# Optimization experiments

Hardware: AMD Instinct MI355X
Metric: run time of the kernel (lower is better)

Reference implementation:

```python
import jax, jax.numpy as jnp
import numpy as np

B, S, H, K = 8, 2048, 768, 128
FILTERS = (1, 3, 5)
C = H // len(FILTERS)  # 256 channels per conv, concat -> H
LN_EPS = 1e-05
COS_EPS = 1e-08


def setup_inputs() -> dict:
    key = jax.random.key(0)
    ks = jax.random.split(key, 16)
    mk = lambda k, shape: jax.random.normal(k, shape, dtype=jnp.float32) * 0.02
    return {
        "representation": jax.random.normal(ks[0], (B, S, H), dtype=jnp.float32),
        "src_mask": jnp.ones((B, S), dtype=jnp.float32),
        # conv weights stored as [k, H_in, C_out] for lax 1D conv (torch Conv2d(1,C,(k,H)))
        "enc_conv_w1": mk(ks[1], (1, H, C)),
        "enc_conv_w3": mk(ks[2], (3, H, C)),
        "enc_conv_w5": mk(ks[3], (5, H, C)),
        "ln_g": jnp.ones((H,), jnp.float32),
        "ln_b": jnp.zeros((H,), jnp.float32),
        "enc_lin_w": mk(ks[4], (H, H)),   # torch Linear weight [out,in]
        "enc_tr_w": mk(ks[5], (K, H)),
        "dec_tr_w": mk(ks[6], (H, K)),
        "dec_conv_w1": mk(ks[7], (1, H, C)),
        "dec_conv_w3": mk(ks[8], (3, H, C)),
        "dec_conv_w5": mk(ks[9], (5, H, C)),
        "dec_lin_w": mk(ks[10], (H, H)),
        "out_lin_w": mk(ks[11], (H, H)),
    }


def _multi_conv(x, ws):
    # x: [B, S, H]; each w: [k, H, C]; torch pads (k//2, 0) -> same-length for odd k
    outs = []
    for w in ws:
        k = w.shape[0]
        outs.append(jax.lax.conv_general_dilated(
            x, w, window_strides=(1,), padding=[(k // 2, k // 2)],
            dimension_numbers=("NWC", "WIO", "NWC")))
    return jnp.concatenate(outs, axis=-1)  # [B, S, H]


def _layernorm(x, g, b):
    mu = jnp.mean(x, axis=-1, keepdims=True)
    var = jnp.mean((x - mu) ** 2, axis=-1, keepdims=True)
    return (x - mu) * jax.lax.rsqrt(var + LN_EPS) * g + b


def reference(representation, src_mask, enc_conv_w1, enc_conv_w3, enc_conv_w5,
              ln_g, ln_b, enc_lin_w, enc_tr_w, dec_tr_w,
              dec_conv_w1, dec_conv_w3, dec_conv_w5, dec_lin_w, out_lin_w):
    # ---- AutoEncoder (dropout layers are identity in eval mode) ----
    h = _multi_conv(representation, (enc_conv_w1, enc_conv_w3, enc_conv_w5))
    h = _layernorm(h + representation, ln_g, ln_b)
    h = jnp.tanh(h @ enc_lin_w.T)
    location = h @ enc_tr_w.T            # [B, S, K] (encode_out)
    d = location @ dec_tr_w.T            # [B, S, H]
    d = _multi_conv(d, (dec_conv_w1, dec_conv_w3, dec_conv_w5))
    d = jnp.tanh(d @ dec_lin_w.T)
    decode_out = d @ out_lin_w.T         # [B, S, H]

    # ---- banded pairwise cosine similarity (fuses the torch shift loop) ----
    # torch loop writes dis_matrix[b, i, i+s+1] = cos(loc[b, i+s+1], loc[b, i])
    # for s in range(max_act_len), i.e. the strict upper band of the symmetric
    # pairwise cosine-similarity matrix with offsets 1..max_act_len.
    normed = location / jnp.maximum(
        jnp.sqrt(jnp.sum(location * location, axis=-1, keepdims=True)), COS_EPS)
    sim = jnp.einsum("bid,bjd->bij", normed, normed)  # [B, S, S]
    offs = jnp.arange(S)[None, :] - jnp.arange(S)[:, None]  # j - i
    max_act_len = jnp.max(jnp.sum(src_mask, axis=-1)).astype(jnp.int32)
    band = (offs >= 1) & (offs <= max_act_len)        # [S, S]
    dis_matrix = jnp.where(band[None], sim, 0.0)
    src_dis_mask = src_mask[:, :, None] * src_mask[:, None, :]
    act_dis_tags = band[None].astype(jnp.float32) * src_dis_mask
    return (location, dis_matrix, act_dis_tags, decode_out)
```

## Files before the change

### kernel.cpp

```cpp
#include <hip/hip_runtime.h>

#define B_   8
#define S_   2048
#define H_   768
#define K_   128
#define C_   256
#define SH_  2052
#define MTOK (B_*S_)

typedef __attribute__((ext_vector_type(8))) short short8;
typedef __attribute__((ext_vector_type(4))) float f32x4;

typedef __attribute__((address_space(1))) const void gvoid;
typedef __attribute__((address_space(3))) void lvoid;

__device__ __forceinline__ void gload16(const void* g, void* l) {
    __builtin_amdgcn_global_load_lds((gvoid*)g, (lvoid*)l, 16, 0, 0);
}

__device__ __forceinline__ ushort f2b(float f) {
    union { float f; unsigned u; } v; v.f = f;
    unsigned r = v.u + 0x7fffu + ((v.u >> 16) & 1u);
    return (ushort)(r >> 16);
}
__device__ __forceinline__ float b2f(ushort u) {
    union { unsigned u; float f; } v; v.u = ((unsigned)u) << 16;
    return v.f;
}
__device__ __forceinline__ float fast_tanh(float x) {
    float e = __expf(2.f * x);
    return 1.f - 2.f / (e + 1.f);
}


struct CvtE { const float* src; ushort* dst; int n; int kh; int sld; };

struct PrepP {
    const float* mask; int* Lp; ushort* lh;
    const float* rep;  ushort* xh;
    CvtE e[11];
};

__global__ __launch_bounds__(256) void k_prep(PrepP p) {
    const int tid = threadIdx.x;
    const int y = blockIdx.y;
    if (y == 0) {
        if (blockIdx.x == 0) {
            __shared__ float sh[4];
            float mx = 0.f;
            for (int b = 0; b < B_; ++b) {
                float s = 0.f;
                for (int q = tid; q < 512; q += 256) {
                    const float4 v = ((const float4*)(p.mask + b * S_))[q];
                    s += v.x + v.y + v.z + v.w;
                }
#pragma unroll
                for (int off = 32; off; off >>= 1) s += __shfl_xor(s, off);
                if ((tid & 63) == 0) sh[tid >> 6] = s;
                __syncthreads();
                if (tid == 0) mx = fmaxf(mx, sh[0] + sh[1] + sh[2] + sh[3]);
                __syncthreads();
            }
            if (tid == 0) *p.Lp = (int)mx;
            for (int i = tid; i < B_ * 4 * K_; i += 256) {
                const int b = i >> 9;
                const int rc = i & 511;
                const int rr = rc >> 7;
                const int cc = rc & 127;
                const int row = (rr < 2) ? rr : (2048 + rr);
                p.lh[((size_t)b * SH_ + row) * K_ + cc] = 0;
            }
        } else {
            int i = (blockIdx.x - 1) * 256 + tid;
            const int stride = (gridDim.x - 1) * 256;
            const int n4 = B_ * SH_ * H_ / 4;
            for (; i < n4; i += stride) {
                const int idx = i * 4;
                const int h = idx % H_;
                const int rs = idx / H_;
                const int s = rs % SH_;
                const int b = rs / SH_;
                ushort4 o; o.x = 0; o.y = 0; o.z = 0; o.w = 0;
                if (s >= 2 && s < S_ + 2) {
                    const float4 v = *(const float4*)(p.rep + ((size_t)b * S_ + (s - 2)) * H_ + h);
                    o.x = f2b(v.x); o.y = f2b(v.y); o.z = f2b(v.z); o.w = f2b(v.w);
                }
                *(ushort4*)(p.xh + idx) = o;
            }
        }
    } else {
        const CvtE e = p.e[y - 1];
        int i = blockIdx.x * 256 + tid;
        const int stride = gridDim.x * 256;
        for (; i < e.n; i += stride) {
            if (e.kh) {
                const int c = i / e.kh;
                const int r = i - c * e.kh;
                e.dst[i] = f2b(e.src[r * e.sld + c]);
            } else {
                e.dst[i] = f2b(e.src[i]);
            }
        }
    }
}


struct CompE { const ushort* w; int wld; int woff; ushort* o; int old_; int koff; };
struct CompP { const ushort* dtrT; CompE e[9]; };

__global__ __launch_bounds__(256) void k_compw(CompP p) {
    __shared__ __align__(16) ushort As[128 * 64];
    __shared__ __align__(16) ushort Bs[128 * 64];
    const CompE e = p.e[blockIdx.y];
    const int tid = threadIdx.x;
    const int w = tid >> 6, lane = tid & 63;
    const int l15 = lane & 15, lk = lane >> 4;
    const int wr = w >> 1, wc = w & 1;
    const int n_base = blockIdx.x * 128;
    f32x4 acc[4][4] = {};
    const int srow = lane >> 3;
    const int scol = (lane & 7) * 8;

    for (int kt = 0; kt < 12; ++kt) {
        const int kk = kt << 6;
#pragma unroll
        for (int q = 0; q < 4; ++q) {
            const int r = w * 32 + q * 8;
            gload16(p.dtrT + (size_t)(r + srow) * 768 + kk + scol, As + r * 64);
            gload16(e.w + (size_t)(n_base + r + srow) * e.wld + e.woff + kk + scol, Bs + r * 64);
        }
        __syncthreads();
#pragma unroll
        for (int ks = 0; ks < 2; ++ks) {
            short8 af[4], bfr[4];
#pragma unroll
            for (int i = 0; i < 4; ++i)
                af[i] = *(const short8*)(As + (wr * 64 + i * 16 + l15) * 64 + ks * 32 + 8 * lk);
#pragma unroll
            for (int j = 0; j < 4; ++j)
                bfr[j] = *(const short8*)(Bs + (wc * 64 + j * 16 + l15) * 64 + ks * 32 + 8 * lk);
#pragma unroll
            for (int i = 0; i < 4; ++i)
#pragma unroll
                for (int j = 0; j < 4; ++j)
                    acc[i][j] = __builtin_amdgcn_mfma_f32_16x16x32_bf16(af[i], bfr[j], acc[i][j], 0, 0, 0);
        }
        __syncthreads();
    }
#pragma unroll
    for (int i = 0; i < 4; ++i)
#pragma unroll
        for (int j = 0; j < 4; ++j)
#pragma unroll
            for (int jj = 0; jj < 4; ++jj) {
                const int jr = wr * 64 + i * 16 + 4 * lk + jj;
                const int c  = n_base + wc * 64 + j * 16 + l15;
                e.o[(size_t)c * e.old_ + e.koff + jr] = f2b(acc[i][j][jj]);
            }
}


struct G3P {
    const ushort* A;
    const ushort* W0;
    const ushort* W1;
    const ushort* W2;
    int lda;
    ushort* outB; int ldoB;
    int nMtiles;
};

template<bool DEC>
__global__ __launch_bounds__(512, 2) void g3(G3P p) {
    constexpr int TPT = DEC ? 2 : 12;
    constexpr int LDA = DEC ? 128 : 768;
    constexpr int ASEG = 1024;
    constexpr int BSEG = 2048;
    constexpr int BUFE = (ASEG + BSEG) * 8;
    __shared__ __align__(16) ushort lds[3][BUFE];

    const int tid = threadIdx.x;
    const int w = tid >> 6, lane = tid & 63;
    const int l15 = lane & 15, lk = lane >> 4;
    const int wr = w >> 2, wc = w & 3;
    const int axor = l15 & 7;

    const int nM = p.nMtiles;
    int idx = blockIdx.x;
    int br;
    if (idx < nM) br = 2;
    else if (idx < 2 * nM) { br = 1; idx -= nM; }
    else { br = 0; idx -= 2 * nM; }
    const int m_base = idx * 128;
    const int n_base = br * 256;
    const int nt = TPT * (2 * br + 1);
    const int Ktot = LDA * (2 * br + 1);
    const ushort* Wt = (br == 0) ? p.W0 : (br == 1) ? p.W1 : p.W2;
    const int arow0 = m_base + ((m_base >> 11) << 2) + (2 - br);

    auto stage1 = [&](int kt, int bufi, int q) {
        const int tap = kt / TPT;
        const int h0 = (kt - tap * TPT) << 6;
        if (q < 2) {
            const int seg = q * 512 + tid;
            const int row = seg >> 3;
            const int slot = (seg & 7) ^ (row & 7);
            gload16(p.A + (size_t)(arow0 + tap + row) * LDA + h0 + slot * 8,
                    &lds[bufi][seg * 8]);
        } else {
            const int seg = (q - 2) * 512 + tid;
            const int row = seg >> 3;
            const int slot = (seg & 7) ^ (row & 7);
            gload16(Wt + (size_t)row * Ktot + (kt << 6) + slot * 8,
                    &lds[bufi][ASEG * 8 + seg * 8]);
        }
    };
    auto stage = [&](int kt, int bufi) {
#pragma unroll
        for (int q = 0; q < 6; ++q) stage1(kt, bufi, q);
    };

    f32x4 acc[4][4] = {};

    stage(0, 0);
    stage(1, 1);

    int buf = 0;
    for (int t = 0; t < nt; ++t) {
        const ushort* Ab = &lds[buf][0];
        const ushort* Bb = &lds[buf][ASEG * 8];
        if (t + 1 < nt) asm volatile("s_waitcnt vmcnt(6)" ::: "memory");
        else            asm volatile("s_waitcnt vmcnt(0)" ::: "memory");
        __builtin_amdgcn_sched_barrier(0);
        asm volatile("s_barrier" ::: "memory");
        __builtin_amdgcn_sched_barrier(0);

        int nbuf = buf + 2; if (nbuf >= 3) nbuf -= 3;
        const bool sb = (t + 2 < nt);

#pragma unroll
        for (int ks = 0; ks < 2; ++ks) {
            short8 bq[4], aq[4];
#pragma unroll
            for (int ni = 0; ni < 4; ++ni)
                bq[ni] = *(const short8*)(Bb + (wc * 64 + ni * 16 + l15) * 64 + ((((ks << 2) | lk) ^ axor) << 3));
#pragma unroll
            for (int mi = 0; mi < 4; ++mi)
                aq[mi] = *(const short8*)(Ab + (wr * 64 + mi * 16 + l15) * 64 + ((((ks << 2) | lk) ^ axor) << 3));
            if (sb) { stage1(t + 2, nbuf, 3 * ks); stage1(t + 2, nbuf, 3 * ks + 1); stage1(t + 2, nbuf, 3 * ks + 2); }
            asm volatile("s_waitcnt lgkmcnt(0)" ::: "memory");
            __builtin_amdgcn_sched_barrier(0);
            __builtin_amdgcn_s_setprio(1);
#pragma unroll
            for (int mi = 0; mi < 4; ++mi)
#pragma unroll
                for (int ni = 0; ni < 4; ++ni)
                    acc[mi][ni] = __builtin_amdgcn_mfma_f32_16x16x32_bf16(aq[mi], bq[ni], acc[mi][ni], 0, 0, 0);
            __builtin_amdgcn_s_setprio(0);
            __builtin_amdgcn_sched_barrier(0);
        }
        ++buf; if (buf == 3) buf = 0;
    }

#pragma unroll
    for (int mi = 0; mi < 4; ++mi)
#pragma unroll
        for (int ni = 0; ni < 4; ++ni)
#pragma unroll
            for (int jj = 0; jj < 4; ++jj) {
                const int r = m_base + wr * 64 + mi * 16 + 4 * lk + jj;
                const int n = n_base + wc * 64 + ni * 16 + l15;
                p.outB[(size_t)r * p.ldoB + n] = f2b(acc[mi][ni][jj]);
            }
}


struct G4P {
    const ushort* A;
    const ushort* W;
    int Ktot;
    int lda;
    ushort* outB; int ldoB;
    float*  outF; int ldoF;
    int act;
};

__global__ __launch_bounds__(256, 2) void g4(G4P p) {
    constexpr int ASEG = 1024;
    constexpr int BSEG = 1536;
    __shared__ __align__(16) ushort lds[2][(ASEG + BSEG) * 8];

    const int tid = threadIdx.x;
    const int w = tid >> 6, lane = tid & 63;
    const int l15 = lane & 15, lk = lane >> 4;
    const int wr = w >> 1, wc = w & 1;
    const int axor = l15 & 7;
    const int m_base = blockIdx.x * 128;
    const int n_base = blockIdx.y * 192;
    const int nt = p.Ktot >> 6;

    auto stage = [&](int kt, int bufi) {
        const int kk = kt << 6;
        ushort* Ab = &lds[bufi][0];
        ushort* Bb = &lds[bufi][ASEG * 8];
#pragma unroll
        for (int q = 0; q < 4; ++q) {
            const int seg = q * 256 + tid;
            const int row = seg >> 3;
            const int s = (seg & 7) ^ (row & 7);
            gload16(p.A + (size_t)(m_base + row) * p.lda + kk + s * 8, Ab + seg * 8);
        }
#pragma unroll
        for (int q = 0; q < 6; ++q) {
            const int seg = q * 256 + tid;
            const int row = seg >> 3;
            const int s = (seg & 7) ^ (row & 7);
            gload16(p.W + (size_t)(n_base + row) * p.Ktot + kk + s * 8, Bb + seg * 8);
        }
    };

    f32x4 acc[4][6] = {};

    stage(0, 0);
    stage(1, 1);

    for (int t = 0; t < nt; ++t) {
        const int cur = t & 1;
        const ushort* Ab = &lds[cur][0];
        const ushort* Bb = &lds[cur][ASEG * 8];
        if (t + 1 < nt) asm volatile("s_waitcnt vmcnt(10)" ::: "memory");
        else            asm volatile("s_waitcnt vmcnt(0)" ::: "memory");
        __builtin_amdgcn_sched_barrier(0);
        asm volatile("s_barrier" ::: "memory");
        __builtin_amdgcn_sched_barrier(0);

        short8 af[4][2], bf[6][2];
#pragma unroll
        for (int mi = 0; mi < 4; ++mi)
#pragma unroll
            for (int ks = 0; ks < 2; ++ks)
                af[mi][ks] = *(const short8*)(Ab + (wr * 64 + mi * 16 + l15) * 64 + ((((ks << 2) | lk) ^ axor) << 3));
#pragma unroll
        for (int ni = 0; ni < 6; ++ni)
#pragma unroll
            for (int ks = 0; ks < 2; ++ks)
                bf[ni][ks] = *(const short8*)(Bb + (wc * 96 + ni * 16 + l15) * 64 + ((((ks << 2) | lk) ^ axor) << 3));
        asm volatile("s_waitcnt lgkmcnt(0)" ::: "memory");
        __builtin_amdgcn_sched_barrier(0);
        asm volatile("s_barrier" ::: "memory");
        __builtin_amdgcn_sched_barrier(0);
        if (t + 2 < nt) stage(t + 2, cur);
        __builtin_amdgcn_sched_barrier(0);
        __builtin_amdgcn_s_setprio(1);
#pragma unroll
        for (int mi = 0; mi < 4; ++mi)
#pragma unroll
            for (int ni = 0; ni < 6; ++ni) {
                acc[mi][ni] = __builtin_amdgcn_mfma_f32_16x16x32_bf16(af[mi][0], bf[ni][0], acc[mi][ni], 0, 0, 0);
                acc[mi][ni] = __builtin_amdgcn_mfma_f32_16x16x32_bf16(af[mi][1], bf[ni][1], acc[mi][ni], 0, 0, 0);
            }
        __builtin_amdgcn_s_setprio(0);
        __builtin_amdgcn_sched_barrier(0);
    }

#pragma unroll
    for (int mi = 0; mi < 4; ++mi)
#pragma unroll
        for (int ni = 0; ni < 6; ++ni)
#pragma unroll
            for (int jj = 0; jj < 4; ++jj) {
                const int r = m_base + wr * 64 + mi * 16 + 4 * lk + jj;
                const int n = n_base + wc * 96 + ni * 16 + l15;
                float v = acc[mi][ni][jj];
                if (p.act) v = fast_tanh(v);
                if (p.outF) p.outF[(size_t)r * p.ldoF + n] = v;
                if (p.outB) p.outB[(size_t)r * p.ldoB + n] = f2b(v);
            }
}


struct GLP {
    const ushort* A;
    const ushort* Wt;
    float* outF;
    ushort* outH;
    ushort* outN;
};

__global__ __launch_bounds__(256) void gemm_loc(GLP p) {
    __shared__ __align__(16) ushort As[64 * 64];
    __shared__ __align__(16) ushort Bs[128 * 64];
    __shared__ float rowss[64][2];
    const int tid = threadIdx.x;
    const int w = tid >> 6, lane = tid & 63;
    const int l15 = lane & 15, lk = lane >> 4;
    const int m_base = blockIdx.x * 64;
    const int wr = w >> 1, wc = w & 1;
    f32x4 acc[2][4] = {};
    const int srow = lane >> 3;
    const int scol = (lane & 7) * 8;

    for (int kt = 0; kt < 12; ++kt) {
        const int kk = kt << 6;
#pragma unroll
        for (int q = 0; q < 2; ++q) {
            const int r = w * 16 + q * 8;
            gload16(p.A + (size_t)(m_base + r + srow) * H_ + kk + scol, As + r * 64);
        }
#pragma unroll
        for (int q = 0; q < 4; ++q) {
            const int r = w * 32 + q * 8;
            gload16(p.Wt + (size_t)(r + srow) * H_ + kk + scol, Bs + r * 64);
        }
        __syncthreads();
#pragma unroll
        for (int ks = 0; ks < 2; ++ks) {
            short8 af[2], bfr[4];
#pragma unroll
            for (int i = 0; i < 2; ++i)
                af[i] = *(const short8*)(As + (wr * 32 + i * 16 + l15) * 64 + ks * 32 + 8 * lk);
#pragma unroll
            for (int j = 0; j < 4; ++j)
                bfr[j] = *(const short8*)(Bs + (wc * 64 + j * 16 + l15) * 64 + ks * 32 + 8 * lk);
#pragma unroll
            for (int i = 0; i < 2; ++i)
#pragma unroll
                for (int j = 0; j < 4; ++j)
                    acc[i][j] = __builtin_amdgcn_mfma_f32_16x16x32_bf16(af[i], bfr[j], acc[i][j], 0, 0, 0);
        }
        __syncthreads();
    }

#pragma unroll
    for (int i = 0; i < 2; ++i)
#pragma unroll
        for (int jj = 0; jj < 4; ++jj) {
            float s = acc[i][0][jj] * acc[i][0][jj] + acc[i][1][jj] * acc[i][1][jj]
                    + acc[i][2][jj] * acc[i][2][jj] + acc[i][3][jj] * acc[i][3][jj];
#pragma unroll
            for (int off = 1; off < 16; off <<= 1) s += __shfl_xor(s, off);
            if (l15 == 0) rowss[wr * 32 + i * 16 + 4 * lk + jj][wc] = s;
        }
    __syncthreads();

    const int bb4 = ((m_base >> 11) << 2) + 2;
#pragma unroll
    for (int i = 0; i < 2; ++i)
#pragma unroll
        for (int j = 0; j < 4; ++j)
#pragma unroll
            for (int jj = 0; jj < 4; ++jj) {
                const int lr = wr * 32 + i * 16 + 4 * lk + jj;
                const int r  = m_base + lr;
                const int n  = wc * 64 + j * 16 + l15;
                const float v = acc[i][j][jj];
                const float ss = rowss[lr][0] + rowss[lr][1];
                const float sc = 1.f / fmaxf(sqrtf(ss), 1e-8f);
                p.outF[(size_t)r * K_ + n] = v;
                p.outH[(size_t)(r + bb4) * K_ + n] = f2b(v);
                p.outN[(size_t)r * K_ + n] = f2b(v * sc);
            }
}


__global__ __launch_bounds__(192) void k_ln(const ushort* __restrict__ conv,
                                            const float* __restrict__ rep,
                                            const float* __restrict__ gw,
                                            const float* __restrict__ bw,
                                            ushort* __restrict__ out) {
    const int row = blockIdx.x;
    const int tid = threadIdx.x;
    const int h = tid * 4;
    const ushort4 cv = *(const ushort4*)(conv + (size_t)row * H_ + h);
    const float4  rv = *(const float4*)(rep + (size_t)row * H_ + h);
    float v[4] = { b2f(cv.x) + rv.x, b2f(cv.y) + rv.y, b2f(cv.z) + rv.z, b2f(cv.w) + rv.w };
    float s1 = v[0] + v[1] + v[2] + v[3];
    float s2 = v[0]*v[0] + v[1]*v[1] + v[2]*v[2] + v[3]*v[3];
#pragma unroll
    for (int off = 32; off; off >>= 1) { s1 += __shfl_xor(s1, off); s2 += __shfl_xor(s2, off); }
    __shared__ float sh[6];
    const int wid = tid >> 6, lane = tid & 63;
    if (lane == 0) { sh[wid] = s1; sh[3 + wid] = s2; }
    __syncthreads();
    s1 = sh[0] + sh[1] + sh[2];
    s2 = sh[3] + sh[4] + sh[5];
    const float mu  = s1 * (1.f / H_);
    const float var = s2 * (1.f / H_) - mu * mu;
    const float rs  = rsqrtf(var + 1e-5f);
    const float4 gv = *(const float4*)(gw + h);
    const float4 bv = *(const float4*)(bw + h);
    ushort4 o;
    o.x = f2b((v[0] - mu) * rs * gv.x + bv.x);
    o.y = f2b((v[1] - mu) * rs * gv.y + bv.y);
    o.z = f2b((v[2] - mu) * rs * gv.z + bv.z);
    o.w = f2b((v[3] - mu) * rs * gv.w + bv.w);
    *(ushort4*)(out + (size_t)row * H_ + h) = o;
}


__global__ __launch_bounds__(256) void k_simtags(const ushort* __restrict__ normed,
                                                 const float* __restrict__ mask,
                                                 const int* __restrict__ Lp,
                                                 float* __restrict__ dis,
                                                 float* __restrict__ tags) {
    const int wid = threadIdx.x >> 6, lane = threadIdx.x & 63;
    const int l15 = lane & 15, lk = lane >> 4;
    const int b   = blockIdx.z;
    const int i0b = blockIdx.x * 64;
    const int i0  = i0b + wid * 16;
    const int j0  = blockIdx.y * 64;
    const int L   = *Lp;
    f32x4 acc[4] = {};
    if ((j0 + 63 >= i0b + 1) && (j0 <= i0b + 63 + L)) {
        const ushort* nb = normed + (size_t)b * S_ * K_;
#pragma unroll
        for (int kt = 0; kt < 4; ++kt) {
            const int kk = kt * 32;
            const short8 a = *(const short8*)(nb + (size_t)(i0 + l15) * K_ + kk + 8 * lk);
#pragma unroll
            for (int j = 0; j < 4; ++j) {
                const short8 bfr = *(const short8*)(nb + (size_t)(j0 + j * 16 + l15) * K_ + kk + 8 * lk);
                acc[j] = __builtin_amdgcn_mfma_f32_16x16x32_bf16(a, bfr, acc[j], 0, 0, 0);
            }
        }
    }
    const float* mb = mask + b * S_;
    float* dp = dis  + (size_t)b * S_ * S_;
    float* tp = tags + (size_t)b * S_ * S_;
#pragma unroll
    for (int j = 0; j < 4; ++j) {
#pragma unroll
        for (int jj = 0; jj < 4; ++jj) {
            const int i  = i0 + 4 * lk + jj;
            const int jc = j0 + j * 16 + l15;
            const int d  = jc - i;
            const bool band = (d >= 1 && d <= L);
            dp[(size_t)i * S_ + jc] = band ? acc[j][jj] : 0.f;
            tp[(size_t)i * S_ + jc] = band ? mb[i] * mb[jc] : 0.f;
        }
    }
}


extern "C" void kernel_launch(void* const* d_in, const int* in_sizes, int n_in,
                              void* d_out, int out_size, void* d_ws, size_t ws_size,
                              hipStream_t stream) {
    const float* rep  = (const float*)d_in[0];
    const float* mask = (const float*)d_in[1];
    const float* ew1  = (const float*)d_in[2];
    const float* ew3  = (const float*)d_in[3];
    const float* ew5  = (const float*)d_in[4];
    const float* lng  = (const float*)d_in[5];
    const float* lnb  = (const float*)d_in[6];
    const float* elin = (const float*)d_in[7];
    const float* etr  = (const float*)d_in[8];
    const float* dtr  = (const float*)d_in[9];
    const float* dw1  = (const float*)d_in[10];
    const float* dw3  = (const float*)d_in[11];
    const float* dw5  = (const float*)d_in[12];
    const float* dlin = (const float*)d_in[13];
    const float* olin = (const float*)d_in[14];

    float* out_loc = (float*)d_out;
    float* out_dis = out_loc + (size_t)B_ * S_ * K_;
    float* out_tag = out_dis + (size_t)B_ * S_ * S_;
    float* out_dec = out_tag + (size_t)B_ * S_ * S_;

    char* ws = (char*)d_ws;
    size_t off = 0;
    auto alloc = [&](size_t bytes) -> char* {
        char* p = ws + off;
        off += (bytes + 255) & ~(size_t)255;
        return p;
    };
    int*    Lp    = (int*)alloc(256);
    ushort* Xh    = (ushort*)alloc((size_t)B_ * SH_ * H_ * 2);
    ushort* bufLh = (ushort*)alloc((size_t)B_ * SH_ * K_ * 2);
    ushort* wte1  = (ushort*)alloc((size_t)C_ * 768 * 2);
    ushort* wte3  = (ushort*)alloc((size_t)C_ * 2304 * 2);
    ushort* wte5  = (ushort*)alloc((size_t)C_ * 3840 * 2);
    ushort* wtd1  = (ushort*)alloc((size_t)C_ * 768 * 2);
    ushort* wtd3  = (ushort*)alloc((size_t)C_ * 2304 * 2);
    ushort* wtd5  = (ushort*)alloc((size_t)C_ * 3840 * 2);
    ushort* welin = (ushort*)alloc((size_t)H_ * H_ * 2);
    ushort* wetr  = (ushort*)alloc((size_t)K_ * H_ * 2);
    ushort* dtrT  = (ushort*)alloc((size_t)K_ * H_ * 2);
    ushort* wdlin = (ushort*)alloc((size_t)H_ * H_ * 2);
    ushort* wolin = (ushort*)alloc((size_t)H_ * H_ * 2);
    ushort* wc1   = (ushort*)alloc((size_t)C_ * 128 * 2);
    ushort* wc3   = (ushort*)alloc((size_t)C_ * 384 * 2);
    ushort* wc5   = (ushort*)alloc((size_t)C_ * 640 * 2);
    ushort* bufB  = (ushort*)alloc((size_t)MTOK * H_ * 2);
    ushort* bufC  = (ushort*)alloc((size_t)MTOK * H_ * 2);
    ushort* bufD  = (ushort*)alloc((size_t)MTOK * H_ * 2);
    ushort* bufN  = (ushort*)alloc((size_t)MTOK * K_ * 2);
    if (ws_size < off) return;

    PrepP pp;
    pp.mask = mask; pp.Lp = Lp; pp.lh = bufLh;
    pp.rep = rep; pp.xh = Xh;
    pp.e[0]  = { ew1,  wte1, 768 * C_,  768,  C_ };
    pp.e[1]  = { ew3,  wte3, 2304 * C_, 2304, C_ };
    pp.e[2]  = { ew5,  wte5, 3840 * C_, 3840, C_ };
    pp.e[3]  = { dw1,  wtd1, 768 * C_,  768,  C_ };
    pp.e[4]  = { dw3,  wtd3, 2304 * C_, 2304, C_ };
    pp.e[5]  = { dw5,  wtd5, 3840 * C_, 3840, C_ };
    pp.e[6]  = { elin, welin, H_ * H_, 0, 0 };
    pp.e[7]  = { etr,  wetr,  K_ * H_, 0, 0 };
    pp.e[8]  = { dlin, wdlin, H_ * H_, 0, 0 };
    pp.e[9]  = { olin, wolin, H_ * H_, 0, 0 };
    pp.e[10] = { dtr,  dtrT,  K_ * H_, 768, K_ };
    k_prep<<<dim3(2048, 12), 256, 0, stream>>>(pp);

    {
        CompP cp; cp.dtrT = dtrT;
        cp.e[0] = { wtd1, 768,  0,        wc1, 128, 0 };
        for (int t = 0; t < 3; ++t) cp.e[1 + t] = { wtd3, 2304, t * 768, wc3, 384, t * 128 };
        for (int t = 0; t < 5; ++t) cp.e[4 + t] = { wtd5, 3840, t * 768, wc5, 640, t * 128 };
        k_compw<<<dim3(2, 9), 256, 0, stream>>>(cp);
    }

    {
        G3P p{}; p.A = Xh; p.W0 = wte1; p.W1 = wte3; p.W2 = wte5;
        p.lda = H_; p.outB = bufB; p.ldoB = H_; p.nMtiles = MTOK / 128;
        g3<false><<<3 * (MTOK / 128), 512, 0, stream>>>(p);
    }
    k_ln<<<MTOK, 192, 0, stream>>>(bufB, rep, lng, lnb, bufC);
    {
        G4P p{}; p.A = bufC; p.W = welin; p.Ktot = H_; p.lda = H_;
        p.outB = bufD; p.ldoB = H_; p.act = 1;
        g4<<<dim3(MTOK / 128, H_ / 192), 256, 0, stream>>>(p);
    }
    {
        GLP p{ bufD, wetr, out_loc, bufLh, bufN };
        gemm_loc<<<MTOK / 64, 256, 0, stream>>>(p);
    }
    {
        G3P p{}; p.A = bufLh; p.W0 = wc1; p.W1 = wc3; p.W2 = wc5;
        p.lda = K_; p.outB = bufB; p.ldoB = H_; p.nMtiles = MTOK / 128;
        g3<true><<<3 * (MTOK / 128), 512, 0, stream>>>(p);
    }
    {
        G4P p{}; p.A = bufB; p.W = wdlin; p.Ktot = H_; p.lda = H_;
        p.outB = bufC; p.ldoB = H_; p.act = 1;
        g4<<<dim3(MTOK / 128, H_ / 192), 256, 0, stream>>>(p);
    }
    {
        G4P p{}; p.A = bufC; p.W = wolin; p.Ktot = H_; p.lda = H_;
        p.outF = out_dec; p.ldoF = H_;
        g4<<<dim3(MTOK / 128, H_ / 192), 256, 0, stream>>>(p);
    }
    k_simtags<<<dim3(S_ / 64, S_ / 64, B_), 256, 0, stream>>>(bufN, mask, Lp, out_dis, out_tag);
}
```

Before: 371.0 us.

## Fold decoder multi-width conv into one zero-padded GEMM and swizzle block order

The three decoder convolution branches (widths 1, 3, 5 over K=128) are packed into a single zero-padded weight matrix of 768x640. They then run through the generic g4 GEMM, which reads overlapping A rows from the halo-padded location buffer, so a row stride of 128 with K=640 covers the five taps. This replaces the per-branch g3 launch and its uneven work per branch with one balanced tiling, at the cost of extra multiplies on the zero-padded taps. Block indices in g3, g4 and gemm_loc are also permuted so that co-scheduled blocks touch more spread-out M tiles, aiming for better cache and channel locality.

```diff
diff --git a/kernel.cpp b/kernel.cpp
--- a/kernel.cpp
+++ b/kernel.cpp
@@ -38,7 +38,7 @@
 struct PrepP {
     const float* mask; int* Lp; ushort* lh;
     const float* rep;  ushort* xh;
-    CvtE e[11];
+    CvtE e[12];
 };
 
 __global__ __launch_bounds__(256) void k_prep(PrepP p) {
@@ -93,7 +93,9 @@
         int i = blockIdx.x * 256 + tid;
         const int stride = gridDim.x * 256;
         for (; i < e.n; i += stride) {
-            if (e.kh) {
+            if (e.kh < 0) {
+                e.dst[i] = 0;
+            } else if (e.kh) {
                 const int c = i / e.kh;
                 const int r = i - c * e.kh;
                 e.dst[i] = f2b(e.src[r * e.sld + c]);
@@ -170,10 +172,9 @@
     int nMtiles;
 };
 
-template<bool DEC>
 __global__ __launch_bounds__(512, 2) void g3(G3P p) {
-    constexpr int TPT = DEC ? 2 : 12;
-    constexpr int LDA = DEC ? 128 : 768;
+    constexpr int TPT = 12;
+    constexpr int LDA = 768;
     constexpr int ASEG = 1024;
     constexpr int BSEG = 2048;
     constexpr int BUFE = (ASEG + BSEG) * 8;
@@ -191,6 +192,7 @@
     if (idx < nM) br = 2;
     else if (idx < 2 * nM) { br = 1; idx -= nM; }
     else { br = 0; idx -= 2 * nM; }
+    idx = (idx & 7) * 16 + (idx >> 3);
     const int m_base = idx * 128;
     const int n_base = br * 256;
     const int nt = TPT * (2 * br + 1);
@@ -283,6 +285,7 @@
     ushort* outB; int ldoB;
     float*  outF; int ldoF;
     int act;
+    int haloA;
 };
 
 __global__ __launch_bounds__(256, 2) void g4(G4P p) {
@@ -295,9 +298,11 @@
     const int l15 = lane & 15, lk = lane >> 4;
     const int wr = w >> 1, wc = w & 1;
     const int axor = l15 & 7;
-    const int m_base = blockIdx.x * 128;
+    const int bx = (blockIdx.x & 7) * 16 + (blockIdx.x >> 3);
+    const int m_base = bx * 128;
     const int n_base = blockIdx.y * 192;
     const int nt = p.Ktot >> 6;
+    const int abase = p.haloA ? (m_base + ((m_base >> 11) << 2)) : m_base;
 
     auto stage = [&](int kt, int bufi) {
         const int kk = kt << 6;
@@ -308,7 +313,7 @@
             const int seg = q * 256 + tid;
             const int row = seg >> 3;
             const int s = (seg & 7) ^ (row & 7);
-            gload16(p.A + (size_t)(m_base + row) * p.lda + kk + s * 8, Ab + seg * 8);
+            gload16(p.A + (size_t)(abase + row) * p.lda + kk + s * 8, Ab + seg * 8);
         }
 #pragma unroll
         for (int q = 0; q < 6; ++q) {
@@ -394,7 +399,8 @@
     const int tid = threadIdx.x;
     const int w = tid >> 6, lane = tid & 63;
     const int l15 = lane & 15, lk = lane >> 4;
-    const int m_base = blockIdx.x * 64;
+    const int bx = (blockIdx.x & 7) * 32 + (blockIdx.x >> 3);
+    const int m_base = bx * 64;
     const int wr = w >> 1, wc = w & 1;
     f32x4 acc[2][4] = {};
     const int srow = lane >> 3;
@@ -587,9 +593,7 @@
     ushort* dtrT  = (ushort*)alloc((size_t)K_ * H_ * 2);
     ushort* wdlin = (ushort*)alloc((size_t)H_ * H_ * 2);
     ushort* wolin = (ushort*)alloc((size_t)H_ * H_ * 2);
-    ushort* wc1   = (ushort*)alloc((size_t)C_ * 128 * 2);
-    ushort* wc3   = (ushort*)alloc((size_t)C_ * 384 * 2);
-    ushort* wc5   = (ushort*)alloc((size_t)C_ * 640 * 2);
+    ushort* Wc    = (ushort*)alloc((size_t)H_ * 640 * 2);
     ushort* bufB  = (ushort*)alloc((size_t)MTOK * H_ * 2);
     ushort* bufC  = (ushort*)alloc((size_t)MTOK * H_ * 2);
     ushort* bufD  = (ushort*)alloc((size_t)MTOK * H_ * 2);
@@ -610,20 +614,23 @@
     pp.e[8]  = { dlin, wdlin, H_ * H_, 0, 0 };
     pp.e[9]  = { olin, wolin, H_ * H_, 0, 0 };
     pp.e[10] = { dtr,  dtrT,  K_ * H_, 768, K_ };
-    k_prep<<<dim3(2048, 12), 256, 0, stream>>>(pp);
+    pp.e[11] = { nullptr, Wc, H_ * 640, -1, 0 };
+    k_prep<<<dim3(2048, 13), 256, 0, stream>>>(pp);
 
     {
         CompP cp; cp.dtrT = dtrT;
-        cp.e[0] = { wtd1, 768,  0,        wc1, 128, 0 };
-        for (int t = 0; t < 3; ++t) cp.e[1 + t] = { wtd3, 2304, t * 768, wc3, 384, t * 128 };
-        for (int t = 0; t < 5; ++t) cp.e[4 + t] = { wtd5, 3840, t * 768, wc5, 640, t * 128 };
+        cp.e[0] = { wtd1, 768,  0, Wc + (size_t)0 * 640,   640, 2 * 128 };
+        for (int t = 0; t < 3; ++t)
+            cp.e[1 + t] = { wtd3, 2304, t * 768, Wc + (size_t)256 * 640, 640, (1 + t) * 128 };
+        for (int t = 0; t < 5; ++t)
+            cp.e[4 + t] = { wtd5, 3840, t * 768, Wc + (size_t)512 * 640, 640, t * 128 };
         k_compw<<<dim3(2, 9), 256, 0, stream>>>(cp);
     }
 
     {
         G3P p{}; p.A = Xh; p.W0 = wte1; p.W1 = wte3; p.W2 = wte5;
         p.lda = H_; p.outB = bufB; p.ldoB = H_; p.nMtiles = MTOK / 128;
-        g3<false><<<3 * (MTOK / 128), 512, 0, stream>>>(p);
+        g3<<<3 * (MTOK / 128), 512, 0, stream>>>(p);
     }
     k_ln<<<MTOK, 192, 0, stream>>>(bufB, rep, lng, lnb, bufC);
     {
@@ -636,9 +643,9 @@
         gemm_loc<<<MTOK / 64, 256, 0, stream>>>(p);
     }
     {
-        G3P p{}; p.A = bufLh; p.W0 = wc1; p.W1 = wc3; p.W2 = wc5;
-        p.lda = K_; p.outB = bufB; p.ldoB = H_; p.nMtiles = MTOK / 128;
-        g3<true><<<3 * (MTOK / 128), 512, 0, stream>>>(p);
+        G4P p{}; p.A = bufLh; p.W = Wc; p.Ktot = 640; p.lda = K_;
+        p.outB = bufB; p.ldoB = H_; p.haloA = 1;
+        g4<<<dim3(MTOK / 128, H_ / 192), 256, 0, stream>>>(p);
     }
     {
         G4P p{}; p.A = bufB; p.W = wdlin; p.Ktot = H_; p.lda = H_;
```

Result: no change. 374.9 us (+1.1%).
